# Kernel tuning notes

Measured on AMD Instinct MI355X. Metric: run time of the kernel, lower is better.

## Reference

```python
import jax, jax.numpy as jnp
import numpy as np

BS, T, D, H = 2500, 400, 16, 32  # nodes(batch), time steps, input_dim, hidden_dim


def _xavier(key, shape):
    fan_in, fan_out = shape[0], shape[1]
    lim = np.sqrt(6.0 / (fan_in + fan_out)).astype(np.float32)
    return jax.random.uniform(key, shape, jnp.float32, -lim, lim)


def setup_inputs() -> dict:
    key = jax.random.key(0)
    ks = jax.random.split(key, 6)
    x = jax.random.normal(ks[0], (BS, T, D), jnp.float32)
    # dense adjacency over the batch/node dim, scaled small like a normalized river-network adjacency
    adj = jax.random.normal(ks[1], (BS, BS), jnp.float32) * 0.01
    return {
        "x": x,
        "adj": adj,
        "W_ih": _xavier(ks[2], (D, 4 * H)),
        "W_hh": _xavier(ks[3], (H, 4 * H)),
        "b": jnp.zeros((4 * H,), jnp.float32),
        "W_q": _xavier(ks[4], (H, H)),
        "b_q": jnp.zeros((H,), jnp.float32),
        "W_d": _xavier(ks[5], (H, 1)),
        "b_d": jnp.zeros((1,), jnp.float32),
    }


def reference(x, adj, W_ih, W_hh, b, W_q, b_q, W_d, b_d):
    # RGCN_Multi.forward_task0 (eval mode: dropouts are identity).
    HS = W_q.shape[0]
    bs = x.shape[0]

    def step(carry, x_t):
        h, c = carry  # [bs, HS] each
        gates = x_t @ W_ih + h @ W_hh + b  # [bs, 4*HS]
        i_t = jax.nn.sigmoid(gates[:, :HS])
        f_t = jax.nn.sigmoid(gates[:, HS:2 * HS])
        g_t = jnp.tanh(gates[:, 2 * HS:3 * HS])
        o_t = jax.nn.sigmoid(gates[:, 3 * HS:])
        q_t = jnp.tanh(h @ W_q + b_q)          # [bs, HS]
        c = f_t * (c + adj @ q_t) + i_t * g_t  # graph aggregation fused into cell state
        h = o_t * jnp.tanh(c)
        return (h, c), h

    h0 = jnp.zeros((bs, HS), x.dtype)
    (_, _), hs = jax.lax.scan(step, (h0, h0), jnp.swapaxes(x, 0, 1))  # hs: [T, bs, HS]
    hidden_seq = jnp.swapaxes(hs, 0, 1)  # [bs, T, HS]
    return hidden_seq @ W_d + b_d        # Task0Module dense head -> [bs, T, 1]
```

## Files before the change

kernel.cpp:

```cpp
#include <hip/hip_runtime.h>
#include <hip/hip_bf16.h>

#define BSN   2500
#define TT    400
#define DIN   16
#define HS    32
#define G4    128
#define NBLK  157
#define NTHR  512
#define ROWS  16
#define MPAD  (NBLK * ROWS)
#define KPAD  2528
#define NCHUNK 79
#define HPAD  36
#define FLAGSTRIDE 16

#define REGUS   (NCHUNK * 512)

#define WS_FLAGS_OFF  0
#define WS_ADJ_OFF    16384
#define WS_ADJ_BYTES  ((size_t)MPAD * KPAD * 2)
#define WS_QT_OFF     (WS_ADJ_OFF + WS_ADJ_BYTES)
#define QT_SLICE      ((size_t)HS * KPAD)
#define WS_NEED_RING  (WS_QT_OFF + (size_t)TT * QT_SLICE * 2)

typedef __attribute__((ext_vector_type(8))) __bf16 bf16x8;
typedef __attribute__((ext_vector_type(4))) float floatx4;
typedef unsigned short ushort_t;
typedef unsigned long long u64_t;

__device__ __forceinline__ float sigmoid_fast(float v) {
    return 1.0f / (1.0f + __expf(-v));
}
__device__ __forceinline__ float tanh_fast(float v) {
    float e = __expf(2.0f * v);
    return 1.0f - 2.0f / (e + 1.0f);
}
__device__ __forceinline__ ushort_t f2bf(float f) {
    union { float f; unsigned u; } x; x.f = f;
    unsigned r = x.u + 0x7fffu + ((x.u >> 16) & 1u);
    return (ushort_t)(r >> 16);
}

__global__ void sentinel(float* __restrict__ out, int n) {
    int i = blockIdx.x * blockDim.x + threadIdx.x;
    if (i < n) out[i] = 12345.0f;
}

__global__ void prep(const float* __restrict__ adj, ushort_t* __restrict__ adj_bf,
                     ushort_t* __restrict__ qT, unsigned* __restrict__ flags) {
    const size_t idx0 = (size_t)blockIdx.x * blockDim.x + threadIdx.x;
    const size_t stride = (size_t)gridDim.x * blockDim.x;
    const size_t total = (size_t)MPAD * KPAD;
    for (size_t idx = idx0; idx < total; idx += stride) {
        int r = (int)(idx / KPAD);
        int k = (int)(idx - (size_t)r * KPAD);
        float v = (r < BSN && k < BSN) ? adj[(size_t)r * BSN + k] : 0.0f;
        adj_bf[idx] = f2bf(v);
    }
    for (size_t idx = idx0; idx < 2 * QT_SLICE; idx += stride) qT[idx] = 0;
    if (idx0 < NBLK * FLAGSTRIDE) flags[idx0] = 0;
}

#define QLOAD(p) __hip_atomic_load((p), __ATOMIC_RELAXED, __HIP_MEMORY_SCOPE_AGENT)

template<int NC>
__device__ __forceinline__ void p2_frag(const ushort_t* __restrict__ afrag,
                                        const ushort_t* __restrict__ q0,
                                        const ushort_t* __restrict__ q1,
                                        const int cbeg,
                                        floatx4& acc0, floatx4& acc1) {
    bf16x8 b0[NC], b1[NC];
#pragma unroll
    for (int i = 0; i < NC; i++) {
        b0[i] = *(const bf16x8*)(q0 + (size_t)(cbeg + i) * 512);
        b1[i] = *(const bf16x8*)(q1 + (size_t)(cbeg + i) * 512);
    }
#pragma unroll
    for (int i = 0; i < NC; i++) {
        bf16x8 av = *(const bf16x8*)(afrag + (size_t)(cbeg + i) * 512);
        acc0 = __builtin_amdgcn_mfma_f32_16x16x32_bf16(av, b0[i], acc0, 0, 0, 0);
        acc1 = __builtin_amdgcn_mfma_f32_16x16x32_bf16(av, b1[i], acc1, 0, 0, 0);
    }
}

template<bool RING>
__global__ void __launch_bounds__(NTHR, 2) rgcn_main(
    const float* __restrict__ x,
    const float* __restrict__ W_ih,
    const float* __restrict__ W_hh,
    const float* __restrict__ bias,
    const float* __restrict__ W_q,
    const float* __restrict__ b_q,
    const float* __restrict__ W_d,
    const float* __restrict__ b_d,
    const ushort_t* __restrict__ adj_bf,
    ushort_t* __restrict__ qT,
    unsigned* __restrict__ flags,
    float* __restrict__ out)
{
    const int tid  = threadIdx.x;
    const int blk  = blockIdx.x;
    const int base = blk * ROWS;
    const int wv   = tid >> 6;
    const int lane = tid & 63;

    __shared__ __align__(16) ushort_t adj_lds[NCHUNK * 512];
    __shared__ __align__(16) float x_lds[ROWS][DIN];
    __shared__ __align__(16) float h_lds[ROWS][HPAD];
    __shared__ __align__(16) float c_lds[ROWS][HPAD];
    __shared__ __align__(16) float q_lds[ROWS][HPAD];
    __shared__ __align__(16) float out_lds[ROWS][16];
    __shared__ float gates_lds[ROWS][G4];
    __shared__ float part[2][7][2][16][16];

    const int u2 = tid & 63;
    float wih0[DIN], wih1[DIN], whh0[HS], whh1[HS];
#pragma unroll
    for (int k = 0; k < DIN; k++) {
        wih0[k] = W_ih[k*G4 + u2]; wih1[k] = W_ih[k*G4 + u2 + 64];
        asm volatile("" : "+v"(wih0[k]), "+v"(wih1[k]));
    }
#pragma unroll
    for (int k = 0; k < HS; k++) {
        whh0[k] = W_hh[k*G4 + u2]; whh1[k] = W_hh[k*G4 + u2 + 64];
        asm volatile("" : "+v"(whh0[k]), "+v"(whh1[k]));
    }
    const float bu0 = bias[u2], bu1 = bias[u2 + 64];

    const int hq = tid & 31;
    const int nq = tid >> 5;
    const float bqv = b_q[hq];
    const float wdv = W_d[hq];
    const float bdv = b_d[0];
    float c_reg = 0.0f;

    float wqr[HS];
#pragma unroll
    for (int k = 0; k < HS; k++) {
        wqr[k] = W_q[k*HS + hq];
        asm volatile("" : "+v"(wqr[k]));
    }

    int cbeg = 0, nch = 0;
    if (wv >= 1 && wv <= 3)      { cbeg = (wv - 1) * 12;      nch = 12; }
    else if (wv >= 4 && wv <= 6) { cbeg = 36 + (wv - 4) * 11; nch = 11; }
    else if (wv == 7)            { cbeg = 69;                 nch = 10; }
    const int pollbase = 2 * cbeg;
    const int pollcnt  = (wv == 0) ? 0
                       : ((2 * (cbeg + nch) < NBLK ? 2 * (cbeg + nch) : NBLK) - pollbase);
    const unsigned* pollf = flags + (size_t)(pollbase + lane) * FLAGSTRIDE;
    const bool dopoll = (wv >= 1) && (lane < pollcnt);

    int xnode = -1, xk = lane & 15;
    if (wv >= 1 && lane < 32)                   xnode = 2*wv + (lane >> 4);
    else if ((wv == 1 || wv == 2) && lane < 48) xnode = wv - 1;
    const int xgn = base + xnode;
    const bool xok = (xnode >= 0) && (xgn < BSN);

    {
        const int n16_per_row = KPAD / 8;
        for (int i = tid; i < ROWS * n16_per_row; i += NTHR) {
            int r = i / n16_per_row, o = i - r * n16_per_row;
            int c = o >> 2, kb = o & 3;
            *(uint4*)(adj_lds + (size_t)c * 512 + (size_t)(kb * 16 + r) * 8) =
                ((const uint4*)(adj_bf + (size_t)(base + r) * KPAD))[o];
        }
    }
    for (int i = tid; i < ROWS * HPAD; i += NTHR) {
        (&h_lds[0][0])[i] = 0.0f;
        (&c_lds[0][0])[i] = 0.0f;
    }
    __syncthreads();

    auto do_gates = [&](int nn) {
        float a0 = bu0, a1 = bu1;
#pragma unroll
        for (int k4 = 0; k4 < DIN/4; k4++) {
            float4 xv = *(const float4*)&x_lds[nn][k4*4];
            a0 = fmaf(xv.x, wih0[k4*4+0], a0); a1 = fmaf(xv.x, wih1[k4*4+0], a1);
            a0 = fmaf(xv.y, wih0[k4*4+1], a0); a1 = fmaf(xv.y, wih1[k4*4+1], a1);
            a0 = fmaf(xv.z, wih0[k4*4+2], a0); a1 = fmaf(xv.z, wih1[k4*4+2], a1);
            a0 = fmaf(xv.w, wih0[k4*4+3], a0); a1 = fmaf(xv.w, wih1[k4*4+3], a1);
        }
#pragma unroll
        for (int k4 = 0; k4 < HS/4; k4++) {
            float4 hv = *(const float4*)&h_lds[nn][k4*4];
            a0 = fmaf(hv.x, whh0[k4*4+0], a0); a1 = fmaf(hv.x, whh1[k4*4+0], a1);
            a0 = fmaf(hv.y, whh0[k4*4+1], a0); a1 = fmaf(hv.y, whh1[k4*4+1], a1);
            a0 = fmaf(hv.z, whh0[k4*4+2], a0); a1 = fmaf(hv.z, whh1[k4*4+2], a1);
            a0 = fmaf(hv.w, whh0[k4*4+3], a0); a1 = fmaf(hv.w, whh1[k4*4+3], a1);
        }
        gates_lds[nn][u2]      = sigmoid_fast(a0);
        gates_lds[nn][u2 + 64] = (u2 < HS) ? tanh_fast(a1) : sigmoid_fast(a1);
    };

    auto do_p1b = [&]() {
        float a = bqv;
#pragma unroll
        for (int k4 = 0; k4 < HS/4; k4++) {
            float4 hv = *(const float4*)&h_lds[nq][k4*4];
            a = fmaf(hv.x, wqr[k4*4+0], a);
            a = fmaf(hv.y, wqr[k4*4+1], a);
            a = fmaf(hv.z, wqr[k4*4+2], a);
            a = fmaf(hv.w, wqr[k4*4+3], a);
        }
        q_lds[nq][hq] = tanh_fast(a);
    };

    if constexpr (RING) {
        float xreg = xok ? x[(size_t)xgn * (TT*DIN) + xk] : 0.0f;

        const int pc    = blk >> 1;
        const int phalf = blk & 1;
        const int preg  = lane >> 5;
        const int pidx  = lane & 31;
        const int ph    = (pidx & 15) + 16 * preg;
        const int pln0  = (pidx >> 4) * 8;

        for (int t = 0; t < TT; t++) {
            const unsigned phase = (unsigned)(t + 1);
            const ushort_t* qslice = qT + (size_t)t * QT_SLICE;

            do_p1b();
            __syncthreads();

            if (wv == 0) {
                unsigned d[4];
#pragma unroll
                for (int j = 0; j < 4; j++) {
                    const int n0 = pln0 + 2*j;
                    d[j] = (unsigned)f2bf(q_lds[n0][ph])
                         | ((unsigned)f2bf(q_lds[n0 + 1][ph]) << 16);
                }
                u64_t v0 = (u64_t)d[0] | ((u64_t)d[1] << 32);
                u64_t v1 = (u64_t)d[2] | ((u64_t)d[3] << 32);
                u64_t* dst = (u64_t*)((ushort_t*)qslice + (size_t)preg * REGUS
                                      + (size_t)pc * 512 + phalf * 256 + pidx * 8);
                __hip_atomic_store(dst,     v0, __ATOMIC_RELAXED, __HIP_MEMORY_SCOPE_AGENT);
                __hip_atomic_store(dst + 1, v1, __ATOMIC_RELAXED, __HIP_MEMORY_SCOPE_AGENT);
                asm volatile("s_waitcnt vmcnt(0)" ::: "memory");
                if (lane == 0) {
                    __hip_atomic_store(flags + blk * FLAGSTRIDE, phase,
                                       __ATOMIC_RELAXED, __HIP_MEMORY_SCOPE_AGENT);
                }
                if (t >= 16 && (t & 15) == 0) {
                    const int node = lane >> 2, qtr = lane & 3;
                    const int gn = base + node;
                    if (gn < BSN) {
                        *(float4*)(out + (size_t)gn * TT + (t - 16) + qtr * 4) =
                            *(const float4*)&out_lds[node][qtr * 4];
                    }
                }
            } else {
                if (xnode >= 0) {
                    x_lds[xnode][xk] = xok ? xreg : 0.0f;
                    const int tn = (t + 1 < TT) ? (t + 1) : (TT - 1);
                    if (xok) xreg = x[(size_t)xgn * (TT*DIN) + (size_t)tn * DIN + xk];
                }
                do_gates(2*wv);
                do_gates(2*wv + 1);
                if (wv <= 2) do_gates(wv - 1);
            }

            if (dopoll) {
                while (QLOAD(pollf) < phase) {}
            }

            if (wv >= 1) {
                floatx4 acc0 = {0.f,0.f,0.f,0.f}, acc1 = {0.f,0.f,0.f,0.f};
                const int mcol = lane & 15;
                const int kb   = lane >> 4;
                const ushort_t* afrag = adj_lds + (size_t)lane * 8;
                const ushort_t* q0 = qslice + (size_t)lane * 8;
                const ushort_t* q1 = qslice + (size_t)REGUS + (size_t)lane * 8;
                if (wv <= 3)      p2_frag<12>(afrag, q0, q1, cbeg, acc0, acc1);
                else if (wv <= 6) p2_frag<11>(afrag, q0, q1, cbeg, acc0, acc1);
                else              p2_frag<10>(afrag, q0, q1, cbeg, acc0, acc1);
#pragma unroll
                for (int r = 0; r < 4; r++) {
                    part[t & 1][wv - 1][0][kb*4 + r][mcol] = acc0[r];
                    part[t & 1][wv - 1][1][kb*4 + r][mcol] = acc1[r];
                }
            }
            __syncthreads();

            {
                const int ntile = hq >> 4, col = hq & 15;
                float agg = 0.0f;
#pragma unroll
                for (int j = 0; j < 7; j++) agg += part[t & 1][j][ntile][nq][col];
                float iv = gates_lds[nq][hq];
                float fv = gates_lds[nq][HS + hq];
                float gv = gates_lds[nq][2*HS + hq];
                float ov = gates_lds[nq][3*HS + hq];
                float cv = fv * (c_reg + agg) + iv * gv;
                float hvv = ov * tanh_fast(cv);
                c_reg = cv;
                h_lds[nq][hq] = hvv;
                float p = hvv * wdv;
                p += __shfl_xor(p, 16);
                p += __shfl_xor(p, 8);
                p += __shfl_xor(p, 4);
                p += __shfl_xor(p, 2);
                p += __shfl_xor(p, 1);
                if (hq == 0) out_lds[nq][t & 15] = p + bdv;
            }
        }
        __syncthreads();
        if (wv == 0) {
            const int node = lane >> 2, qtr = lane & 3;
            const int gn = base + node;
            if (gn < BSN) {
                *(float4*)(out + (size_t)gn * TT + (TT - 16) + qtr * 4) =
                    *(const float4*)&out_lds[node][qtr * 4];
            }
        }
    } else {
        for (int t = 0; t < TT; t++) {
            const unsigned phase = (unsigned)(t + 1);
            ushort_t* qbuf = qT + (size_t)(t & 1) * QT_SLICE;

            do_p1b();
            __syncthreads();

            if (tid < 256) {
                const int h0 = tid >> 3;
                const int pr = tid & 7;
                unsigned val = (unsigned)f2bf(q_lds[2*pr][h0])
                             | ((unsigned)f2bf(q_lds[2*pr + 1][h0]) << 16);
                unsigned* p = (unsigned*)(qbuf + (size_t)h0 * KPAD + base) + pr;
                __hip_atomic_store(p, val, __ATOMIC_RELAXED, __HIP_MEMORY_SCOPE_AGENT);
            }
            if (lane < 32) {
                const int node = 2*wv + (lane >> 4), k = lane & 15;
                const int gn = base + node;
                x_lds[node][k] = (gn < BSN) ? x[(size_t)gn * (TT*DIN) + (size_t)t*DIN + k] : 0.0f;
            }
            do_gates(2*wv);
            do_gates(2*wv + 1);
            asm volatile("s_waitcnt vmcnt(0)" ::: "memory");
            __syncthreads();
            if (tid == 0) {
                __hip_atomic_store(flags + blk * FLAGSTRIDE, phase,
                                   __ATOMIC_RELAXED, __HIP_MEMORY_SCOPE_AGENT);
            }
            if (tid < NBLK) {
                const unsigned* f = flags + tid * FLAGSTRIDE;
                while (QLOAD(f) < phase) {}
            }
            __syncthreads();

            {
                floatx4 acc0 = {0.f,0.f,0.f,0.f}, acc1 = {0.f,0.f,0.f,0.f};
                const int mcol = lane & 15;
                const int kb   = lane >> 4;
                const ushort_t* afrag = adj_lds + (size_t)lane * 8;
                const u64_t* q0 = (const u64_t*)(qbuf + (size_t)mcol        * KPAD) + kb*2;
                const u64_t* q1 = (const u64_t*)(qbuf + (size_t)(mcol + 16) * KPAD) + kb*2;
                const int cb2 = wv * 10;
                const int ce2 = (cb2 + 10 < NCHUNK) ? cb2 + 10 : NCHUNK;
                for (int c = cb2; c < ce2; c++) {
                    bf16x8 av = *(const bf16x8*)(afrag + (size_t)c * 512);
                    union { u64_t u[2]; bf16x8 v; } b0, b1;
                    b0.u[0] = QLOAD(q0 + c*8);
                    b0.u[1] = QLOAD(q0 + c*8 + 1);
                    b1.u[0] = QLOAD(q1 + c*8);
                    b1.u[1] = QLOAD(q1 + c*8 + 1);
                    acc0 = __builtin_amdgcn_mfma_f32_16x16x32_bf16(av, b0.v, acc0, 0, 0, 0);
                    acc1 = __builtin_amdgcn_mfma_f32_16x16x32_bf16(av, b1.v, acc1, 0, 0, 0);
                }
                float* pw = &part[0][0][0][0][0] + (size_t)wv * 2 * 16 * 16;
#pragma unroll
                for (int r = 0; r < 4; r++) {
                    pw[(0*16 + kb*4 + r) * 16 + mcol] = acc0[r];
                    pw[(1*16 + kb*4 + r) * 16 + mcol] = acc1[r];
                }
            }
            __syncthreads();

            {
                const int ntile = hq >> 4, col = hq & 15;
                float agg = 0.0f;
                const float* pbase = &part[0][0][0][0][0];
#pragma unroll
                for (int w = 0; w < 8; w++) {
                    agg += pbase[(size_t)w * 2 * 16 * 16 + (ntile*16 + nq) * 16 + col];
                }
                float iv = gates_lds[nq][hq];
                float fv = gates_lds[nq][HS + hq];
                float gv = gates_lds[nq][2*HS + hq];
                float ov = gates_lds[nq][3*HS + hq];
                float cv = fv * (c_lds[nq][hq] + agg) + iv * gv;
                float hv = ov * tanh_fast(cv);
                c_lds[nq][hq] = cv;
                h_lds[nq][hq] = hv;
                float p = hv * wdv;
                p += __shfl_xor(p, 16);
                p += __shfl_xor(p, 8);
                p += __shfl_xor(p, 4);
                p += __shfl_xor(p, 2);
                p += __shfl_xor(p, 1);
                if (hq == 0) {
                    int gn = base + nq;
                    if (gn < BSN) out[(size_t)gn * TT + t] = p + bdv;
                }
            }
            __syncthreads();
        }
    }
}

extern "C" void kernel_launch(void* const* d_in, const int* in_sizes, int n_in,
                              void* d_out, int out_size, void* d_ws, size_t ws_size,
                              hipStream_t stream) {
    const float* x    = (const float*)d_in[0];
    const float* adj  = (const float*)d_in[1];
    const float* W_ih = (const float*)d_in[2];
    const float* W_hh = (const float*)d_in[3];
    const float* bias = (const float*)d_in[4];
    const float* W_q  = (const float*)d_in[5];
    const float* b_q  = (const float*)d_in[6];
    const float* W_d  = (const float*)d_in[7];
    const float* b_d  = (const float*)d_in[8];
    float* out = (float*)d_out;

    unsigned* flags = (unsigned*)((char*)d_ws + WS_FLAGS_OFF);
    ushort_t* adj_bf = (ushort_t*)((char*)d_ws + WS_ADJ_OFF);
    ushort_t* qT = (ushort_t*)((char*)d_ws + WS_QT_OFF);

    const bool ring = (ws_size >= WS_NEED_RING);

    hipLaunchKernelGGL(sentinel, dim3((out_size + 255) / 256), dim3(256), 0, stream,
                       out, out_size);
    hipLaunchKernelGGL(prep, dim3(2048), dim3(256), 0, stream, adj, adj_bf, qT, flags);

    const ushort_t* adj_bf_c = adj_bf;
    void* args[] = {
        (void*)&x, (void*)&W_ih, (void*)&W_hh, (void*)&bias, (void*)&W_q,
        (void*)&b_q, (void*)&W_d, (void*)&b_d, (void*)&adj_bf_c, (void*)&qT,
        (void*)&flags, (void*)&out
    };
    if (ring) {
        hipLaunchCooperativeKernel((void*)&rgcn_main<true>, dim3(NBLK), dim3(NTHR),
                                   args, 0, stream);
    } else {
        hipLaunchCooperativeKernel((void*)&rgcn_main<false>, dim3(NBLK), dim3(NTHR),
                                   args, 0, stream);
    }
}
```

Baseline: 1.796 ms.

## Poll producer flags with ballot and load q chunks as they become ready

The previous code had every wave spin until all its producer flags were set before loading any q chunks. The new code polls inside the fragment loader, uses a wave ballot, and loads each chunk as soon as both of its producer blocks have published. The q tile is now packed straight into bf16 in LDS in fragment order, so wave 0 can publish it with a single vector read. Wave 0 also takes over the gate work for nodes 0-1, which were previously spread across waves 1-2. This is meant to overlap waiting on remote blocks with loading q, and to shorten the critical publish path, at the cost of a more complex polling loop.

```diff
diff --git a/kernel.cpp b/kernel.cpp
--- a/kernel.cpp
+++ b/kernel.cpp
@@ -65,16 +65,30 @@
 #define QLOAD(p) __hip_atomic_load((p), __ATOMIC_RELAXED, __HIP_MEMORY_SCOPE_AGENT)
 
 template<int NC>
-__device__ __forceinline__ void p2_frag(const ushort_t* __restrict__ afrag,
-                                        const ushort_t* __restrict__ q0,
-                                        const ushort_t* __restrict__ q1,
-                                        const int cbeg,
-                                        floatx4& acc0, floatx4& acc1) {
+__device__ __forceinline__ void p2_ballot(const ushort_t* __restrict__ afrag,
+                                          const ushort_t* __restrict__ q0,
+                                          const ushort_t* __restrict__ q1,
+                                          const int cbeg,
+                                          const unsigned* __restrict__ pollf,
+                                          const bool dopoll,
+                                          const unsigned phase,
+                                          floatx4& acc0, floatx4& acc1) {
     bf16x8 b0[NC], b1[NC];
-#pragma unroll
-    for (int i = 0; i < NC; i++) {
-        b0[i] = *(const bf16x8*)(q0 + (size_t)(cbeg + i) * 512);
-        b1[i] = *(const bf16x8*)(q1 + (size_t)(cbeg + i) * 512);
+    unsigned done = 0;
+    const unsigned full = (1u << NC) - 1u;
+    while (done != full) {
+        bool rdy = (!dopoll) || (QLOAD(pollf) >= phase);
+        u64_t bal = __ballot(rdy);
+        asm volatile("" ::: "memory");
+#pragma unroll
+        for (int i = 0; i < NC; i++) {
+            if (!((done >> i) & 1u) &&
+                ((bal >> (2*i)) & 1ull) && ((bal >> (2*i + 1)) & 1ull)) {
+                b0[i] = *(const bf16x8*)(q0 + (size_t)(cbeg + i) * 512);
+                b1[i] = *(const bf16x8*)(q1 + (size_t)(cbeg + i) * 512);
+                done |= 1u << i;
+            }
+        }
     }
 #pragma unroll
     for (int i = 0; i < NC; i++) {
@@ -106,6 +120,7 @@
     const int lane = tid & 63;
 
     __shared__ __align__(16) ushort_t adj_lds[NCHUNK * 512];
+    __shared__ __align__(16) ushort_t q_pack[512];
     __shared__ __align__(16) float x_lds[ROWS][DIN];
     __shared__ __align__(16) float h_lds[ROWS][HPAD];
     __shared__ __align__(16) float c_lds[ROWS][HPAD];
@@ -142,19 +157,21 @@
         asm volatile("" : "+v"(wqr[k]));
     }
 
-    int cbeg = 0, nch = 0;
-    if (wv >= 1 && wv <= 3)      { cbeg = (wv - 1) * 12;      nch = 12; }
-    else if (wv >= 4 && wv <= 6) { cbeg = 36 + (wv - 4) * 11; nch = 11; }
-    else if (wv == 7)            { cbeg = 69;                 nch = 10; }
+    const int qp_idx = (hq >> 4) * 256 + (((hq & 15) | ((nq >> 3) << 4)) * 8) + (nq & 7);
+
+    int cbeg = 0;
+    if (wv >= 1 && wv <= 3)      cbeg = (wv - 1) * 12;
+    else if (wv >= 4 && wv <= 6) cbeg = 36 + (wv - 4) * 11;
+    else if (wv == 7)            cbeg = 69;
+    const int nch = (wv == 0) ? 0 : ((wv <= 3) ? 12 : ((wv <= 6) ? 11 : 10));
     const int pollbase = 2 * cbeg;
     const int pollcnt  = (wv == 0) ? 0
                        : ((2 * (cbeg + nch) < NBLK ? 2 * (cbeg + nch) : NBLK) - pollbase);
-    const unsigned* pollf = flags + (size_t)(pollbase + lane) * FLAGSTRIDE;
+    const unsigned* pollf = flags + (size_t)(pollbase + (lane < pollcnt ? lane : 0)) * FLAGSTRIDE;
     const bool dopoll = (wv >= 1) && (lane < pollcnt);
 
-    int xnode = -1, xk = lane & 15;
-    if (wv >= 1 && lane < 32)                   xnode = 2*wv + (lane >> 4);
-    else if ((wv == 1 || wv == 2) && lane < 48) xnode = wv - 1;
+    const int xnode = (lane < 32) ? (2*wv + (lane >> 4)) : -1;
+    const int xk = lane & 15;
     const int xgn = base + xnode;
     const bool xok = (xnode >= 0) && (xgn < BSN);
 
@@ -195,7 +212,7 @@
         gates_lds[nn][u2 + 64] = (u2 < HS) ? tanh_fast(a1) : sigmoid_fast(a1);
     };
 
-    auto do_p1b = [&]() {
+    auto do_p1b_f32 = [&]() {
         float a = bqv;
 #pragma unroll
         for (int k4 = 0; k4 < HS/4; k4++) {
@@ -215,35 +232,44 @@
         const int phalf = blk & 1;
         const int preg  = lane >> 5;
         const int pidx  = lane & 31;
-        const int ph    = (pidx & 15) + 16 * preg;
-        const int pln0  = (pidx >> 4) * 8;
 
         for (int t = 0; t < TT; t++) {
             const unsigned phase = (unsigned)(t + 1);
             const ushort_t* qslice = qT + (size_t)t * QT_SLICE;
 
-            do_p1b();
+            {
+                float a = bqv;
+#pragma unroll
+                for (int k4 = 0; k4 < HS/4; k4++) {
+                    float4 hv = *(const float4*)&h_lds[nq][k4*4];
+                    a = fmaf(hv.x, wqr[k4*4+0], a);
+                    a = fmaf(hv.y, wqr[k4*4+1], a);
+                    a = fmaf(hv.z, wqr[k4*4+2], a);
+                    a = fmaf(hv.w, wqr[k4*4+3], a);
+                }
+                q_pack[qp_idx] = f2bf(tanh_fast(a));
+            }
             __syncthreads();
 
             if (wv == 0) {
-                unsigned d[4];
-#pragma unroll
-                for (int j = 0; j < 4; j++) {
-                    const int n0 = pln0 + 2*j;
-                    d[j] = (unsigned)f2bf(q_lds[n0][ph])
-                         | ((unsigned)f2bf(q_lds[n0 + 1][ph]) << 16);
-                }
-                u64_t v0 = (u64_t)d[0] | ((u64_t)d[1] << 32);
-                u64_t v1 = (u64_t)d[2] | ((u64_t)d[3] << 32);
+                union { bf16x8 v; u64_t u[2]; } fr;
+                fr.v = *(const bf16x8*)(q_pack + preg * 256 + pidx * 8);
                 u64_t* dst = (u64_t*)((ushort_t*)qslice + (size_t)preg * REGUS
                                       + (size_t)pc * 512 + phalf * 256 + pidx * 8);
-                __hip_atomic_store(dst,     v0, __ATOMIC_RELAXED, __HIP_MEMORY_SCOPE_AGENT);
-                __hip_atomic_store(dst + 1, v1, __ATOMIC_RELAXED, __HIP_MEMORY_SCOPE_AGENT);
+                __hip_atomic_store(dst,     fr.u[0], __ATOMIC_RELAXED, __HIP_MEMORY_SCOPE_AGENT);
+                __hip_atomic_store(dst + 1, fr.u[1], __ATOMIC_RELAXED, __HIP_MEMORY_SCOPE_AGENT);
                 asm volatile("s_waitcnt vmcnt(0)" ::: "memory");
                 if (lane == 0) {
                     __hip_atomic_store(flags + blk * FLAGSTRIDE, phase,
                                        __ATOMIC_RELAXED, __HIP_MEMORY_SCOPE_AGENT);
                 }
+                if (xnode >= 0) {
+                    x_lds[xnode][xk] = xok ? xreg : 0.0f;
+                    const int tn = (t + 1 < TT) ? (t + 1) : (TT - 1);
+                    if (xok) xreg = x[(size_t)xgn * (TT*DIN) + (size_t)tn * DIN + xk];
+                }
+                do_gates(0);
+                do_gates(1);
                 if (t >= 16 && (t & 15) == 0) {
                     const int node = lane >> 2, qtr = lane & 3;
                     const int gn = base + node;
@@ -260,23 +286,19 @@
                 }
                 do_gates(2*wv);
                 do_gates(2*wv + 1);
-                if (wv <= 2) do_gates(wv - 1);
-            }
-
-            if (dopoll) {
-                while (QLOAD(pollf) < phase) {}
-            }
-
-            if (wv >= 1) {
+
                 floatx4 acc0 = {0.f,0.f,0.f,0.f}, acc1 = {0.f,0.f,0.f,0.f};
                 const int mcol = lane & 15;
                 const int kb   = lane >> 4;
                 const ushort_t* afrag = adj_lds + (size_t)lane * 8;
                 const ushort_t* q0 = qslice + (size_t)lane * 8;
                 const ushort_t* q1 = qslice + (size_t)REGUS + (size_t)lane * 8;
-                if (wv <= 3)      p2_frag<12>(afrag, q0, q1, cbeg, acc0, acc1);
-                else if (wv <= 6) p2_frag<11>(afrag, q0, q1, cbeg, acc0, acc1);
-                else              p2_frag<10>(afrag, q0, q1, cbeg, acc0, acc1);
+                if (wv <= 3)
+                    p2_ballot<12>(afrag, q0, q1, cbeg, pollf, dopoll, phase, acc0, acc1);
+                else if (wv <= 6)
+                    p2_ballot<11>(afrag, q0, q1, cbeg, pollf, dopoll, phase, acc0, acc1);
+                else
+                    p2_ballot<10>(afrag, q0, q1, cbeg, pollf, dopoll, phase, acc0, acc1);
 #pragma unroll
                 for (int r = 0; r < 4; r++) {
                     part[t & 1][wv - 1][0][kb*4 + r][mcol] = acc0[r];
@@ -321,7 +343,7 @@
             const unsigned phase = (unsigned)(t + 1);
             ushort_t* qbuf = qT + (size_t)(t & 1) * QT_SLICE;
 
-            do_p1b();
+            do_p1b_f32();
             __syncthreads();
 
             if (tid < 256) {
```

Result: slower. 2.046 ms (+14.0%).
